# Kernel optimization log

Hardware: AMD Instinct MI355X
Metric: run time of the kernel (lower is better)

The kernel has to match this reference:

```python
import jax, jax.numpy as jnp
import numpy as np
import math

B, S, D, H, F = 4, 1024, 1024, 16, 4096
DH = D // H
NEG = -1000000.0  # matches masked_fill value in MaskedSoftmax
EPS = 1e-5        # torch LayerNorm default


def layer_norm(x, g, b):
    m = jnp.mean(x, axis=-1, keepdims=True)
    v = jnp.mean((x - m) ** 2, axis=-1, keepdims=True)
    return (x - m) * jax.lax.rsqrt(v + EPS) * g + b


def mha(q_in, k_in, v_in, Wq, bq, Wk, bk, Wv, bv, Wo, bo, mask):
    # mask: broadcastable to [B, H, Sq, Sk]; True = keep
    Bq, Sq, _ = q_in.shape
    Sk = k_in.shape[1]
    Q = (q_in @ Wq + bq).reshape(Bq, Sq, H, DH).transpose(0, 2, 1, 3)
    K = (k_in @ Wk + bk).reshape(Bq, Sk, H, DH).transpose(0, 2, 1, 3)
    V = (v_in @ Wv + bv).reshape(Bq, Sk, H, DH).transpose(0, 2, 1, 3)
    scores = jnp.einsum('bhqd,bhkd->bhqk', Q, K) / math.sqrt(DH)
    scores = jnp.where(mask, scores, NEG)
    A = jax.nn.softmax(scores, axis=-1)
    out = jnp.einsum('bhqk,bhkd->bhqd', A, V)
    out = out.transpose(0, 2, 1, 3).reshape(Bq, Sq, D)
    return out @ Wo + bo


def setup_inputs() -> dict:
    key = jax.random.key(0)
    ks = jax.random.split(key, 16)
    w = lambda k, shp: (jax.random.normal(k, shp, dtype=jnp.float32) * 0.02)
    inp = {
        'X': jax.random.normal(ks[0], (B, S, D), dtype=jnp.float32),
        'enc_outputs': jax.random.normal(ks[1], (B, S, D), dtype=jnp.float32),
        'enc_valid_lens': jax.random.randint(ks[2], (B,), 1, S + 1),
        # self-attention
        'Wq1': w(ks[3], (D, D)), 'bq1': jnp.zeros((D,), jnp.float32),
        'Wk1': w(ks[4], (D, D)), 'bk1': jnp.zeros((D,), jnp.float32),
        'Wv1': w(ks[5], (D, D)), 'bv1': jnp.zeros((D,), jnp.float32),
        'Wo1': w(ks[6], (D, D)), 'bo1': jnp.zeros((D,), jnp.float32),
        'g1': jnp.ones((D,), jnp.float32), 'be1': jnp.zeros((D,), jnp.float32),
        # cross-attention
        'Wq2': w(ks[7], (D, D)), 'bq2': jnp.zeros((D,), jnp.float32),
        'Wk2': w(ks[8], (D, D)), 'bk2': jnp.zeros((D,), jnp.float32),
        'Wv2': w(ks[9], (D, D)), 'bv2': jnp.zeros((D,), jnp.float32),
        'Wo2': w(ks[10], (D, D)), 'bo2': jnp.zeros((D,), jnp.float32),
        'g2': jnp.ones((D,), jnp.float32), 'be2': jnp.zeros((D,), jnp.float32),
        # FFN
        'Wf1': w(ks[11], (D, F)), 'bf1': jnp.zeros((F,), jnp.float32),
        'Wf2': w(ks[12], (F, D)), 'bf2': jnp.zeros((D,), jnp.float32),
        'g3': jnp.ones((D,), jnp.float32), 'be3': jnp.zeros((D,), jnp.float32),
    }
    return inp


def reference(X, enc_outputs, enc_valid_lens,
              Wq1, bq1, Wk1, bk1, Wv1, bv1, Wo1, bo1, g1, be1,
              Wq2, bq2, Wk2, bk2, Wv2, bv2, Wo2, bo2, g2, be2,
              Wf1, bf1, Wf2, bf2, g3, be3):
    # training mode, first decode step: key_values = X, causal dec mask
    idx = jnp.arange(S)
    causal = (idx[None, :] <= idx[:, None])[None, None]          # [1,1,S,S]
    cross = (idx[None, :] < enc_valid_lens[:, None])[:, None, None, :]  # [B,1,1,S]

    X2 = mha(X, X, X, Wq1, bq1, Wk1, bk1, Wv1, bv1, Wo1, bo1, causal)
    Y = layer_norm(X2 + X, g1, be1)
    Y2 = mha(Y, enc_outputs, enc_outputs, Wq2, bq2, Wk2, bk2, Wv2, bv2, Wo2, bo2, cross)
    Z = layer_norm(Y2 + Y, g2, be2)
    ffn = jax.nn.relu(Z @ Wf1 + bf1) @ Wf2 + bf2
    return layer_norm(ffn + Z, g3, be3)
```

## Files before the change

kernel.cpp:

```cpp
#include <hip/hip_runtime.h>
#include <stdint.h>

typedef unsigned short u16;
typedef __bf16 bf16x8 __attribute__((ext_vector_type(8)));
typedef float f32x4 __attribute__((ext_vector_type(4)));

#define BB 4
#define SS 1024
#define DD 1024
#define HH 16
#define DHH 64
#define FF 4096
#define NEGV -1000000.0f
#define LOG2E 1.4426950408889634f

__device__ __forceinline__ u16 f2b(float f) {
    uint32_t u = __float_as_uint(f);
    u += 0x7fff + ((u >> 16) & 1);
    return (u16)(u >> 16);
}
__device__ __forceinline__ float b2f(u16 u) {
    return __uint_as_float(((uint32_t)u) << 16);
}
__device__ __forceinline__ float exp2_raw(float x) {
    float r;
    asm volatile("v_exp_f32 %0, %1" : "=v"(r) : "v"(x));
    return r;
}
__device__ __forceinline__ void async16(const void* gp, void* lp) {
    auto g = reinterpret_cast<const __attribute__((address_space(1))) uint32_t*>(
        reinterpret_cast<uintptr_t>(gp));
    auto l = reinterpret_cast<__attribute__((address_space(3))) uint32_t*>(
        reinterpret_cast<uintptr_t>(lp));
    __builtin_amdgcn_global_load_lds(g, l, 16, 0, 0);
}

__global__ void cvt_bf16_kernel(const float* __restrict__ in, u16* __restrict__ out, int n4) {
    int i = blockIdx.x * blockDim.x + threadIdx.x;
    if (i >= n4) return;
    float4 v = reinterpret_cast<const float4*>(in)[i];
    ushort4 o;
    o.x = f2b(v.x); o.y = f2b(v.y); o.z = f2b(v.z); o.w = f2b(v.w);
    reinterpret_cast<ushort4*>(out)[i] = o;
}

__global__ void concat_bias_kernel(const float* __restrict__ a, const float* __restrict__ b,
                                   const float* __restrict__ c, float* __restrict__ out) {
    int i = blockIdx.x * 256 + threadIdx.x;
    float v;
    if (i < 1024) v = a[i];
    else if (i < 2048) v = b[i - 1024];
    else v = c[i - 2048];
    out[i] = v;
}

struct W8 { const float* p[8]; };
__global__ void wtrans8_kernel(W8 wp, u16* __restrict__ dst) {
    __shared__ u16 t[64][68];
    const float* W = wp.p[blockIdx.z];
    u16* Wt = dst + (size_t)blockIdx.z * 1024 * 1024;
    int n0 = blockIdx.x * 64, k0 = blockIdx.y * 64;
    int tx = threadIdx.x & 15, ty = threadIdx.x >> 4;
#pragma unroll
    for (int rr = 0; rr < 4; ++rr) {
        int r = ty + rr * 16;
        float4 v = *reinterpret_cast<const float4*>(&W[(size_t)(k0 + r) * 1024 + n0 + tx * 4]);
        ushort4 o;
        o.x = f2b(v.x); o.y = f2b(v.y); o.z = f2b(v.z); o.w = f2b(v.w);
        *reinterpret_cast<ushort4*>(&t[r][tx * 4]) = o;
    }
    __syncthreads();
#pragma unroll
    for (int rr = 0; rr < 4; ++rr) {
        int n = ty + rr * 16;
        ushort4 o;
        o.x = t[tx * 4 + 0][n];
        o.y = t[tx * 4 + 1][n];
        o.z = t[tx * 4 + 2][n];
        o.w = t[tx * 4 + 3][n];
        *reinterpret_cast<ushort4*>(&Wt[(size_t)(n0 + n) * 1024 + k0 + tx * 4]) = o;
    }
}

__global__ void wtrans_kernel(const float* __restrict__ W, u16* __restrict__ Wt, int K, int N) {
    __shared__ u16 t[64][68];
    int n0 = blockIdx.x * 64, k0 = blockIdx.y * 64;
    int tx = threadIdx.x & 15, ty = threadIdx.x >> 4;
#pragma unroll
    for (int rr = 0; rr < 4; ++rr) {
        int r = ty + rr * 16;
        float4 v = *reinterpret_cast<const float4*>(&W[(size_t)(k0 + r) * N + n0 + tx * 4]);
        ushort4 o;
        o.x = f2b(v.x); o.y = f2b(v.y); o.z = f2b(v.z); o.w = f2b(v.w);
        *reinterpret_cast<ushort4*>(&t[r][tx * 4]) = o;
    }
    __syncthreads();
#pragma unroll
    for (int rr = 0; rr < 4; ++rr) {
        int n = ty + rr * 16;
        ushort4 o;
        o.x = t[tx * 4 + 0][n];
        o.y = t[tx * 4 + 1][n];
        o.z = t[tx * 4 + 2][n];
        o.w = t[tx * 4 + 3][n];
        *reinterpret_cast<ushort4*>(&Wt[(size_t)(n0 + n) * K + k0 + tx * 4]) = o;
    }
}

__global__ void vtrans_kernel(const u16* __restrict__ V, int ldv, u16* __restrict__ VT) {
    __shared__ u16 t[32][33];
    int bh = blockIdx.z;
    int b = bh >> 4, h = bh & 15;
    int s0 = blockIdx.x * 32, d0 = blockIdx.y * 32;
    int tx = threadIdx.x, ty = threadIdx.y;
#pragma unroll
    for (int r = 0; r < 32; r += 8)
        t[ty + r][tx] = V[(size_t)(b * SS + s0 + ty + r) * ldv + h * DHH + d0 + tx];
    __syncthreads();
#pragma unroll
    for (int r = 0; r < 32; r += 8)
        VT[(size_t)(bh * DHH + d0 + ty + r) * SS + s0 + tx] = t[tx][ty + r];
}

template<int BM, bool OUT_BF16, bool RELU, int KSPLIT = 1>
__global__ __launch_bounds__(256, 3) void gemm_bt_kernel(
    const u16* __restrict__ A, const u16* __restrict__ Bt,
    const float* __restrict__ bias, void* __restrict__ Cv,
    int M, int N, int K, int qcols, float qscale)
{
    constexpr int MR = BM / 32;
    __shared__ __attribute__((aligned(16))) u16 As[BM][64];
    __shared__ __attribute__((aligned(16))) u16 Bs[128][64];
    const int tid = threadIdx.x;
    const int lane = tid & 63, wid = tid >> 6;
    const int wr = wid >> 1, wc = wid & 1;
    const int m0 = blockIdx.x * BM, n0 = blockIdx.y * 128;
    const int kz = (KSPLIT > 1) ? blockIdx.z : 0;
    const int Kc = K / KSPLIT;
    const int k0 = kz * Kc;
    const int arow = lane & 15;
    const int kseg = (lane >> 4) * 8;
    const int srow = lane >> 3;
    const int scol = ((lane & 7) ^ srow) * 8;
    const int rswz = (arow & 7) << 3;
    const f32x4 z4 = {0.f, 0.f, 0.f, 0.f};

    f32x4 acc[MR][4];
#pragma unroll
    for (int i = 0; i < MR; ++i)
#pragma unroll
        for (int j = 0; j < 4; ++j) acc[i][j] = z4;

    for (int kt = k0; kt < k0 + Kc; kt += 64) {
        __syncthreads();
#pragma unroll
        for (int i = 0; i < MR; ++i) {
            int ch = wid + i * 4;
            async16(&A[(size_t)(m0 + ch * 8 + srow) * K + kt + scol], &As[ch * 8][0]);
        }
#pragma unroll
        for (int i = 0; i < 4; ++i) {
            int ch = wid + i * 4;
            async16(&Bt[(size_t)(n0 + ch * 8 + srow) * K + kt + scol], &Bs[ch * 8][0]);
        }
        __syncthreads();
#pragma unroll
        for (int ks = 0; ks < 2; ++ks) {
            const int cswz = (ks * 32 + kseg) ^ rswz;
            bf16x8 af[MR], bfr[4];
#pragma unroll
            for (int mi = 0; mi < MR; ++mi)
                af[mi] = *reinterpret_cast<const bf16x8*>(&As[wr * (BM / 2) + mi * 16 + arow][cswz]);
#pragma unroll
            for (int ni = 0; ni < 4; ++ni)
                bfr[ni] = *reinterpret_cast<const bf16x8*>(&Bs[wc * 64 + ni * 16 + arow][cswz]);
#pragma unroll
            for (int mi = 0; mi < MR; ++mi)
#pragma unroll
                for (int ni = 0; ni < 4; ++ni)
                    acc[mi][ni] = __builtin_amdgcn_mfma_f32_16x16x32_bf16(af[mi], bfr[ni], acc[mi][ni], 0, 0, 0);
        }
    }
    const int rrow = (lane >> 4) * 4;
#pragma unroll
    for (int mi = 0; mi < MR; ++mi)
#pragma unroll
        for (int ni = 0; ni < 4; ++ni) {
            int col = n0 + wc * 64 + ni * 16 + arow;
            float bv = (kz == 0) ? bias[col] : 0.f;
            float sc = (col < qcols) ? qscale : 1.f;
#pragma unroll
            for (int r = 0; r < 4; ++r) {
                int row = m0 + wr * (BM / 2) + mi * 16 + rrow + r;
                float v = (acc[mi][ni][r] + bv) * sc;
                if (RELU) v = fmaxf(v, 0.f);
                size_t idx = (size_t)kz * M * N + (size_t)row * N + col;
                if (OUT_BF16) ((u16*)Cv)[idx] = f2b(v);
                else          ((float*)Cv)[idx] = v;
            }
        }
}

template<bool OUT_BF16, bool RELU, int KSPLIT = 1>
__global__ __launch_bounds__(512, 2) void gemm256_kernel(
    const u16* __restrict__ A, const u16* __restrict__ Bt,
    const float* __restrict__ bias, void* __restrict__ Cv,
    int M, int N, int K, int qcols, float qscale)
{
    __shared__ __attribute__((aligned(16))) u16 As[2][256][64];
    __shared__ __attribute__((aligned(16))) u16 Bs[2][256][64];
    const int tid = threadIdx.x, lane = tid & 63, wid = tid >> 6;
    const int wr = wid >> 2, wc = wid & 3;
    const int gx = gridDim.x, nwg = gridDim.x * gridDim.y;
    int bid = blockIdx.y * gx + blockIdx.x;
    int swz = (bid & 7) * (nwg >> 3) + (bid >> 3);
    const int m0 = (swz % gx) * 256, n0 = (swz / gx) * 256;
    const int kz = (KSPLIT > 1) ? blockIdx.z : 0;
    const int Kc = K / KSPLIT, k0 = kz * Kc, NT = Kc >> 6;
    const int a = lane & 15, g = lane >> 4;
    const int srow = lane >> 3;
    const int scol = ((lane & 7) ^ srow) * 8;
    const int rswz = (a & 7) << 3;
    const f32x4 z4 = {0.f, 0.f, 0.f, 0.f};

    f32x4 acc[8][4];
#pragma unroll
    for (int i = 0; i < 8; ++i)
#pragma unroll
        for (int j = 0; j < 4; ++j) acc[i][j] = z4;

    auto stageA = [&](int t, int h) {
        int kt = k0 + t * 64;
#pragma unroll
        for (int i = 0; i < 2; ++i) {
            int row = h * 128 + (wid * 2 + i) * 8;
            async16(&A[(size_t)(m0 + row + srow) * K + kt + scol], &As[t & 1][row][0]);
        }
    };
    auto stageB = [&](int t, int h) {
        int kt = k0 + t * 64;
#pragma unroll
        for (int i = 0; i < 2; ++i) {
            int row = h * 128 + (wid * 2 + i) * 8;
            async16(&Bt[(size_t)(n0 + row + srow) * K + kt + scol], &Bs[t & 1][row][0]);
        }
    };

    stageA(0, 0); stageA(0, 1); stageB(0, 0); stageB(0, 1);
    stageA(1, 0); stageA(1, 1); stageB(1, 0); stageB(1, 1);
    asm volatile("s_waitcnt vmcnt(8)" ::: "memory");
    __builtin_amdgcn_s_barrier();
    asm volatile("" ::: "memory");

    for (int t = 0; t < NT; ++t) {
        const int b = t & 1;
        bf16x8 bf[4][2];
#pragma unroll
        for (int p = 0; p < 4; ++p) {
            bf16x8 af[2][2];
#pragma unroll
            for (int m2 = 0; m2 < 2; ++m2)
#pragma unroll
                for (int ks = 0; ks < 2; ++ks)
                    af[m2][ks] = *reinterpret_cast<const bf16x8*>(
                        &As[b][wr * 128 + (p * 2 + m2) * 16 + a][(ks * 32 + g * 8) ^ rswz]);
            if (p == 0) {
#pragma unroll
                for (int ni = 0; ni < 4; ++ni)
#pragma unroll
                    for (int ks = 0; ks < 2; ++ks)
                        bf[ni][ks] = *reinterpret_cast<const bf16x8*>(
                            &Bs[b][wc * 64 + ni * 16 + a][(ks * 32 + g * 8) ^ rswz]);
            }
            if (p == 0 && t >= 1 && t + 1 < NT) stageA(t + 1, 0);
            if (p == 1 && t >= 1 && t + 1 < NT) stageA(t + 1, 1);
            if (p == 2 && t + 2 < NT) stageB(t + 2, 0);
            if (p == 3 && t + 2 < NT) stageB(t + 2, 1);
            asm volatile("" ::: "memory");
            __builtin_amdgcn_s_barrier();
            asm volatile("" ::: "memory");
            __builtin_amdgcn_s_setprio(1);
#pragma unroll
            for (int ks = 0; ks < 2; ++ks)
#pragma unroll
                for (int m2 = 0; m2 < 2; ++m2)
#pragma unroll
                    for (int ni = 0; ni < 4; ++ni)
                        acc[p * 2 + m2][ni] = __builtin_amdgcn_mfma_f32_16x16x32_bf16(
                            af[m2][ks], bf[ni][ks], acc[p * 2 + m2][ni], 0, 0, 0);
            __builtin_amdgcn_s_setprio(0);
        }
        if (t < NT - 1) {
            if (t < NT - 2) asm volatile("s_waitcnt vmcnt(4)" ::: "memory");
            else            asm volatile("s_waitcnt vmcnt(0)" ::: "memory");
            __builtin_amdgcn_s_barrier();
            asm volatile("" ::: "memory");
        }
    }

    const int rrow = g * 4;
#pragma unroll
    for (int mi = 0; mi < 8; ++mi)
#pragma unroll
        for (int ni = 0; ni < 4; ++ni) {
            int col = n0 + wc * 64 + ni * 16 + a;
            float bv = (kz == 0) ? bias[col] : 0.f;
            float sc = (col < qcols) ? qscale : 1.f;
#pragma unroll
            for (int r = 0; r < 4; ++r) {
                int row = m0 + wr * 128 + mi * 16 + rrow + r;
                float v = (acc[mi][ni][r] + bv) * sc;
                if (RELU) v = fmaxf(v, 0.f);
                size_t idx = (size_t)kz * M * N + (size_t)row * N + col;
                if (OUT_BF16) ((u16*)Cv)[idx] = f2b(v);
                else          ((float*)Cv)[idx] = v;
            }
        }
}

__global__ __launch_bounds__(512, 4) void flash_attn_kernel(
    const u16* __restrict__ Q, int ldq, const u16* __restrict__ Kp, int ldk,
    const u16* __restrict__ VT, u16* __restrict__ O,
    const int* __restrict__ vlens, int causal)
{
    __shared__ __attribute__((aligned(16))) u16 Ks[128][64];
    __shared__ __attribute__((aligned(16))) u16 Vs[64][128];
    __shared__ __attribute__((aligned(16))) u16 Ps[128][64];
    const int tid = threadIdx.x, lane = tid & 63, wid = tid >> 6;
    const int bh = blockIdx.x;
    int qb = blockIdx.y;
    if (causal) qb = (bh & 1) ? (7 - qb) : qb;
    const int b = bh >> 4, h = bh & 15;
    const int q0 = qb * 128;
    const int a = lane & 15;
    const int g = lane >> 4;
    const int kseg = g * 8;
    const int srow = lane >> 3;
    const int scol = ((lane & 7) ^ srow) * 8;
    const int vrow = lane >> 4;
    const int rswz = (a & 7) << 3;
    const int vswz = a << 3;
    const f32x4 z4 = {0.f, 0.f, 0.f, 0.f};

    bf16x8 qf[2];
#pragma unroll
    for (int ks = 0; ks < 2; ++ks)
        qf[ks] = *reinterpret_cast<const bf16x8*>(
            &Q[(size_t)(b * SS + q0 + wid * 16 + a) * ldq + h * DHH + ks * 32 + kseg]);

    float m_run = -3e38f, l_run = 0.f;
    f32x4 o[4];
#pragma unroll
    for (int nd = 0; nd < 4; ++nd) o[nd] = z4;

    int vl = causal ? SS : vlens[b];
    int ntiles = causal ? (qb + 1) : ((vl + 127) >> 7);

    for (int kt = 0; kt < ntiles; ++kt) {
        const int kv0 = kt * 128;
        __syncthreads();
#pragma unroll
        for (int i = 0; i < 2; ++i) {
            int ch = wid + i * 8;
            async16(&Kp[(size_t)(b * SS + kv0 + ch * 8 + srow) * ldk + h * DHH + scol], &Ks[ch * 8][0]);
            int cv = wid + i * 8;
            int vs = (cv * 4 + vrow) & 15;
            async16(&VT[(size_t)(bh * DHH + cv * 4 + vrow) * SS + kv0 + ((lane & 15) ^ vs) * 8], &Vs[cv * 4][0]);
        }
        __syncthreads();

        f32x4 st[8];
#pragma unroll
        for (int ni = 0; ni < 8; ++ni) st[ni] = z4;
        __builtin_amdgcn_s_setprio(1);
#pragma unroll
        for (int ks = 0; ks < 2; ++ks) {
            const int cswz = (ks * 32 + kseg) ^ rswz;
            bf16x8 kf[8];
#pragma unroll
            for (int ni = 0; ni < 8; ++ni)
                kf[ni] = *reinterpret_cast<const bf16x8*>(&Ks[ni * 16 + a][cswz]);
#pragma unroll
            for (int ni = 0; ni < 8; ++ni)
                st[ni] = __builtin_amdgcn_mfma_f32_16x16x32_bf16(kf[ni], qf[ks], st[ni], 0, 0, 0);
        }
        __builtin_amdgcn_s_setprio(0);

        bool domask = causal ? (kt == qb) : (kv0 + 128 > vl);
        if (domask) {
            const int qg = q0 + wid * 16 + a;
#pragma unroll
            for (int ni = 0; ni < 8; ++ni)
#pragma unroll
                for (int r = 0; r < 4; ++r) {
                    int cg = kv0 + ni * 16 + 4 * g + r;
                    bool keep = causal ? (cg <= qg) : (cg < vl);
                    if (!keep) st[ni][r] = NEGV;
                }
        }

        float tm = -3e38f;
#pragma unroll
        for (int ni = 0; ni < 8; ++ni)
#pragma unroll
            for (int r = 0; r < 4; ++r) tm = fmaxf(tm, st[ni][r]);
        tm = fmaxf(tm, __shfl_xor(tm, 16));
        tm = fmaxf(tm, __shfl_xor(tm, 32));
        bool need = __any(tm > m_run + 11.0f);
        float corr = 1.f;
        if (need) {
            float nm = fmaxf(m_run, tm);
            corr = exp2_raw(m_run - nm);
            m_run = nm;
        }
        float rs = 0.f;
#pragma unroll
        for (int ni = 0; ni < 8; ++ni)
#pragma unroll
            for (int r = 0; r < 4; ++r) {
                float p = exp2_raw(st[ni][r] - m_run);
                st[ni][r] = p;
                rs += p;
            }
        rs += __shfl_xor(rs, 16);
        rs += __shfl_xor(rs, 32);
        l_run = l_run * corr + rs;

        if (need) {
#pragma unroll
            for (int r = 0; r < 4; ++r) {
                float cr = __shfl(corr, (lane & 48) + 4 * g + r);
#pragma unroll
                for (int nd = 0; nd < 4; ++nd) o[nd][r] *= cr;
            }
        }

#pragma unroll
        for (int hh = 0; hh < 2; ++hh) {
#pragma unroll
            for (int ni4 = 0; ni4 < 4; ++ni4) {
                int ni = hh * 4 + ni4;
                uint2 pw;
                pw.x = (uint32_t)f2b(st[ni][0]) | ((uint32_t)f2b(st[ni][1]) << 16);
                pw.y = (uint32_t)f2b(st[ni][2]) | ((uint32_t)f2b(st[ni][3]) << 16);
                int prow = wid * 16 + a;
                int pcol = (ni4 * 16 + 4 * g) ^ rswz;
                *reinterpret_cast<uint2*>(&Ps[prow][pcol]) = pw;
            }
            __builtin_amdgcn_s_setprio(1);
#pragma unroll
            for (int kk = 0; kk < 2; ++kk) {
                const int kf_ = hh * 2 + kk;
                const int pswz = (kk * 32 + kseg) ^ rswz;
                const int cvswz = (kf_ * 32 + kseg) ^ vswz;
                bf16x8 pa, vb[4];
                pa = *reinterpret_cast<const bf16x8*>(&Ps[wid * 16 + a][pswz]);
#pragma unroll
                for (int nd = 0; nd < 4; ++nd)
                    vb[nd] = *reinterpret_cast<const bf16x8*>(&Vs[nd * 16 + a][cvswz]);
#pragma unroll
                for (int nd = 0; nd < 4; ++nd)
                    o[nd] = __builtin_amdgcn_mfma_f32_16x16x32_bf16(pa, vb[nd], o[nd], 0, 0, 0);
            }
            __builtin_amdgcn_s_setprio(0);
        }
    }

    float il = 1.f / l_run;
#pragma unroll
    for (int r = 0; r < 4; ++r) {
        float ilr = __shfl(il, (lane & 48) + 4 * g + r);
        int row = q0 + wid * 16 + 4 * g + r;
#pragma unroll
        for (int nd = 0; nd < 4; ++nd)
            O[(size_t)(b * SS + row) * DD + h * DHH + nd * 16 + a] = f2b(o[nd][r] * ilr);
    }
}

template<int NP>
__global__ void add_ln_kernel(const u16* __restrict__ P, size_t pstride,
                              const float* __restrict__ R,
                              const float* __restrict__ g, const float* __restrict__ be,
                              float* __restrict__ out32, u16* __restrict__ out16)
{
    __shared__ float red[4][2];
    const int row = blockIdx.x, tid = threadIdx.x;
    const size_t base = (size_t)row * DD;
    float4 vr = *reinterpret_cast<const float4*>(R + base + tid * 4);
    float x0 = vr.x, x1 = vr.y, x2 = vr.z, x3 = vr.w;
#pragma unroll
    for (int p = 0; p < NP; ++p) {
        ushort4 u = *reinterpret_cast<const ushort4*>(P + p * pstride + base + tid * 4);
        x0 += b2f(u.x); x1 += b2f(u.y); x2 += b2f(u.z); x3 += b2f(u.w);
    }
    float s = x0 + x1 + x2 + x3;
    float q = x0 * x0 + x1 * x1 + x2 * x2 + x3 * x3;
#pragma unroll
    for (int off = 32; off; off >>= 1) {
        s += __shfl_xor(s, off);
        q += __shfl_xor(q, off);
    }
    if ((tid & 63) == 0) { red[tid >> 6][0] = s; red[tid >> 6][1] = q; }
    __syncthreads();
    s = red[0][0] + red[1][0] + red[2][0] + red[3][0];
    q = red[0][1] + red[1][1] + red[2][1] + red[3][1];
    float mean = s * (1.f / 1024.f);
    float var = q * (1.f / 1024.f) - mean * mean;
    float rstd = rsqrtf(var + 1e-5f);
    int c = tid * 4;
    float o0 = (x0 - mean) * rstd * g[c + 0] + be[c + 0];
    float o1 = (x1 - mean) * rstd * g[c + 1] + be[c + 1];
    float o2 = (x2 - mean) * rstd * g[c + 2] + be[c + 2];
    float o3 = (x3 - mean) * rstd * g[c + 3] + be[c + 3];
    float4 ov = {o0, o1, o2, o3};
    *reinterpret_cast<float4*>(out32 + base + c) = ov;
    if (out16) {
        ushort4 hv;
        hv.x = f2b(o0); hv.y = f2b(o1); hv.z = f2b(o2); hv.w = f2b(o3);
        *reinterpret_cast<ushort4*>(out16 + base + c) = hv;
    }
}

extern "C" void kernel_launch(void* const* d_in, const int* in_sizes, int n_in,
                              void* d_out, int out_size, void* d_ws, size_t ws_size,
                              hipStream_t stream)
{
    const float* X   = (const float*)d_in[0];
    const float* ENC = (const float*)d_in[1];
    const int*   VL  = (const int*)d_in[2];
    const float* Wq1 = (const float*)d_in[3];  const float* bq1 = (const float*)d_in[4];
    const float* Wk1 = (const float*)d_in[5];  const float* bk1 = (const float*)d_in[6];
    const float* Wv1 = (const float*)d_in[7];  const float* bv1 = (const float*)d_in[8];
    const float* Wo1 = (const float*)d_in[9];  const float* bo1 = (const float*)d_in[10];
    const float* g1  = (const float*)d_in[11]; const float* be1 = (const float*)d_in[12];
    const float* Wq2 = (const float*)d_in[13]; const float* bq2 = (const float*)d_in[14];
    const float* Wk2 = (const float*)d_in[15]; const float* bk2 = (const float*)d_in[16];
    const float* Wv2 = (const float*)d_in[17]; const float* bv2 = (const float*)d_in[18];
    const float* Wo2 = (const float*)d_in[19]; const float* bo2 = (const float*)d_in[20];
    const float* g2  = (const float*)d_in[21]; const float* be2 = (const float*)d_in[22];
    const float* Wf1 = (const float*)d_in[23]; const float* bf1 = (const float*)d_in[24];
    const float* Wf2 = (const float*)d_in[25]; const float* bf2 = (const float*)d_in[26];
    const float* g3  = (const float*)d_in[27]; const float* be3 = (const float*)d_in[28];

    char* ws = (char*)d_ws;
    const size_t MB = 1024 * 1024;
    u16*   XBF  = (u16*)(ws + 0 * MB);
    u16*   ENCB = (u16*)(ws + 8 * MB);
    u16*   WTsq = (u16*)(ws + 16 * MB);
    u16*   WTf1 = (u16*)(ws + 32 * MB);
    u16*   WTf2 = (u16*)(ws + 40 * MB);
    u16*   QKV  = (u16*)(ws + 48 * MB);
    u16*   HF   = (u16*)(ws + 48 * MB);
    u16*   VTb  = (u16*)(ws + 80 * MB);
    u16*   AO   = (u16*)(ws + 88 * MB);
    u16*   P4   = (u16*)(ws + 80 * MB);
    u16*   P16  = (u16*)(ws + 96 * MB);
    float* Y32  = (float*)(ws + 112 * MB);
    u16*   YBF  = (u16*)(ws + 128 * MB);
    float* Z32  = (float*)(ws + 136 * MB);
    u16*   ZBF  = (u16*)(ws + 152 * MB);
    float* B1 = (float*)d_out;
    float* B2 = (float*)d_out + 4096;
    (void)ws_size; (void)in_sizes; (void)n_in; (void)out_size;

    const int M = BB * SS;
    const size_t MN = (size_t)M * DD;
    const float QS = 0.125f * LOG2E;

    cvt_bf16_kernel<<<M * DD / 4 / 256, 256, 0, stream>>>(X, XBF, M * DD / 4);
    cvt_bf16_kernel<<<M * DD / 4 / 256, 256, 0, stream>>>(ENC, ENCB, M * DD / 4);
    concat_bias_kernel<<<12, 256, 0, stream>>>(bq1, bk1, bv1, B1);
    concat_bias_kernel<<<8, 256, 0, stream>>>(bk2, bv2, bv2, B2);
    W8 w8 = {{Wq1, Wk1, Wv1, Wo1, Wq2, Wk2, Wv2, Wo2}};
    wtrans8_kernel<<<dim3(16, 16, 8), 256, 0, stream>>>(w8, WTsq);
    wtrans_kernel<<<dim3(64, 16), 256, 0, stream>>>(Wf1, WTf1, DD, FF);
    wtrans_kernel<<<dim3(16, 64), 256, 0, stream>>>(Wf2, WTf2, FF, DD);

    gemm256_kernel<true, false><<<dim3(16, 12), 512, 0, stream>>>(XBF, WTsq, B1, QKV, M, 3072, DD, 1024, QS);
    vtrans_kernel<<<dim3(32, 2, 64), dim3(32, 8), 0, stream>>>(QKV + 2048, 3072, VTb);
    flash_attn_kernel<<<dim3(64, 8), 512, 0, stream>>>(QKV, 3072, QKV + 1024, 3072, VTb, AO, VL, 1);
    gemm_bt_kernel<128, true, false, 2><<<dim3(32, 8, 2), 256, 0, stream>>>(AO, WTsq + 3u * 1024 * 1024, bo1, P16, M, DD, DD, 0, 1.f);
    add_ln_kernel<2><<<M, 256, 0, stream>>>(P16, MN, X, g1, be1, Y32, YBF);

    gemm_bt_kernel<64, true, false><<<dim3(64, 8), 256, 0, stream>>>(YBF, WTsq + 4u * 1024 * 1024, bq2, XBF, M, DD, DD, 1024, QS);
    gemm_bt_kernel<128, true, false><<<dim3(32, 16), 256, 0, stream>>>(ENCB, WTsq + 5u * 1024 * 1024, B2, QKV, M, 2048, DD, 0, 1.f);
    vtrans_kernel<<<dim3(32, 2, 64), dim3(32, 8), 0, stream>>>(QKV + 1024, 2048, VTb);
    flash_attn_kernel<<<dim3(64, 8), 512, 0, stream>>>(XBF, 1024, QKV, 2048, VTb, AO, VL, 0);
    gemm_bt_kernel<128, true, false, 2><<<dim3(32, 8, 2), 256, 0, stream>>>(AO, WTsq + 7u * 1024 * 1024, bo2, P16, M, DD, DD, 0, 1.f);
    add_ln_kernel<2><<<M, 256, 0, stream>>>(P16, MN, Y32, g2, be2, Z32, ZBF);

    gemm256_kernel<true, true><<<dim3(16, 16), 512, 0, stream>>>(ZBF, WTf1, bf1, HF, M, FF, DD, 0, 1.f);
    gemm256_kernel<true, false, 4><<<dim3(16, 4, 4), 512, 0, stream>>>(HF, WTf2, bf2, P4, M, DD, FF, 0, 1.f);
    add_ln_kernel<4><<<M, 256, 0, stream>>>(P4, MN, Z32, g3, be3, (float*)d_out, nullptr);
}
```

Before: 316.7 us.

## Restructure GEMM main loop into two-tile unrolled pipeline with explicit waits

Rewrites the 256x256 GEMM k-loop to process two k-tiles per iteration with eight phases. The schedule of async global-to-LDS loads changes: A is now staged one tile ahead and B two tiles ahead. An explicit lgkmcnt wait and sched_barrier come before the MFMAs, and a barrier follows every phase. The goal is to overlap loads with MFMA work better and to stop the compiler from interleaving LDS reads and MFMAs. The cost is more barriers per tile. Reusing the A buffer one tile ahead may also race, and NT must be even.

```diff
diff --git a/kernel.cpp b/kernel.cpp
--- a/kernel.cpp
+++ b/kernel.cpp
@@ -216,7 +216,7 @@
     int swz = (bid & 7) * (nwg >> 3) + (bid >> 3);
     const int m0 = (swz % gx) * 256, n0 = (swz / gx) * 256;
     const int kz = (KSPLIT > 1) ? blockIdx.z : 0;
-    const int Kc = K / KSPLIT, k0 = kz * Kc, NT = Kc >> 6;
+    const int Kc = K / KSPLIT, k0 = kz * Kc, NT = Kc >> 6, NI = NT >> 1;
     const int a = lane & 15, g = lane >> 4;
     const int srow = lane >> 3;
     const int scol = ((lane & 7) ^ srow) * 8;
@@ -247,52 +247,62 @@
     };
 
     stageA(0, 0); stageA(0, 1); stageB(0, 0); stageB(0, 1);
-    stageA(1, 0); stageA(1, 1); stageB(1, 0); stageB(1, 1);
-    asm volatile("s_waitcnt vmcnt(8)" ::: "memory");
+    stageB(1, 0); stageB(1, 1);
+    asm volatile("s_waitcnt vmcnt(4)" ::: "memory");
     __builtin_amdgcn_s_barrier();
     asm volatile("" ::: "memory");
 
-    for (int t = 0; t < NT; ++t) {
-        const int b = t & 1;
+    for (int i = 0; i < NI; ++i) {
+        const int t0 = 2 * i, t1 = 2 * i + 1;
         bf16x8 bf[4][2];
 #pragma unroll
-        for (int p = 0; p < 4; ++p) {
+        for (int p = 1; p <= 8; ++p) {
+            const int buf = (p > 4) ? 1 : 0;
+            const int q = (p - 1) & 3;
             bf16x8 af[2][2];
 #pragma unroll
             for (int m2 = 0; m2 < 2; ++m2)
 #pragma unroll
                 for (int ks = 0; ks < 2; ++ks)
                     af[m2][ks] = *reinterpret_cast<const bf16x8*>(
-                        &As[b][wr * 128 + (p * 2 + m2) * 16 + a][(ks * 32 + g * 8) ^ rswz]);
-            if (p == 0) {
+                        &As[buf][wr * 128 + (q * 2 + m2) * 16 + a][(ks * 32 + g * 8) ^ rswz]);
+            if (q == 0) {
 #pragma unroll
                 for (int ni = 0; ni < 4; ++ni)
 #pragma unroll
                     for (int ks = 0; ks < 2; ++ks)
                         bf[ni][ks] = *reinterpret_cast<const bf16x8*>(
-                            &Bs[b][wc * 64 + ni * 16 + a][(ks * 32 + g * 8) ^ rswz]);
-            }
-            if (p == 0 && t >= 1 && t + 1 < NT) stageA(t + 1, 0);
-            if (p == 1 && t >= 1 && t + 1 < NT) stageA(t + 1, 1);
-            if (p == 2 && t + 2 < NT) stageB(t + 2, 0);
-            if (p == 3 && t + 2 < NT) stageB(t + 2, 1);
+                            &Bs[buf][wc * 64 + ni * 16 + a][(ks * 32 + g * 8) ^ rswz]);
+            }
+            if (p == 1)                { stageA(t1, 0); stageA(t1, 1); }
+            if (p == 2 && t0 + 2 < NT) stageB(t0 + 2, 0);
+            if (p == 3 && t0 + 2 < NT) stageB(t0 + 2, 1);
+            if (p == 5 && t0 + 2 < NT) { stageA(t0 + 2, 0); stageA(t0 + 2, 1); }
+            if (p == 6 && t1 + 2 < NT) stageB(t1 + 2, 0);
+            if (p == 7 && t1 + 2 < NT) stageB(t1 + 2, 1);
             asm volatile("" ::: "memory");
             __builtin_amdgcn_s_barrier();
+            asm volatile("s_waitcnt lgkmcnt(0)" ::: "memory");
+            __builtin_amdgcn_sched_barrier(0);
+            __builtin_amdgcn_s_setprio(1);
+#pragma unroll
+            for (int ks = 0; ks < 2; ++ks)
+#pragma unroll
+                for (int m2 = 0; m2 < 2; ++m2)
+#pragma unroll
+                    for (int ni = 0; ni < 4; ++ni)
+                        acc[q * 2 + m2][ni] = __builtin_amdgcn_mfma_f32_16x16x32_bf16(
+                            af[m2][ks], bf[ni][ks], acc[q * 2 + m2][ni], 0, 0, 0);
+            __builtin_amdgcn_s_setprio(0);
+            if (p == 4) {
+                if (t0 + 2 < NT) asm volatile("s_waitcnt vmcnt(4)" ::: "memory");
+                else             asm volatile("s_waitcnt vmcnt(0)" ::: "memory");
+            }
+            if (p == 8) {
+                if (t1 + 2 < NT) asm volatile("s_waitcnt vmcnt(4)" ::: "memory");
+                else             asm volatile("s_waitcnt vmcnt(0)" ::: "memory");
+            }
             asm volatile("" ::: "memory");
-            __builtin_amdgcn_s_setprio(1);
-#pragma unroll
-            for (int ks = 0; ks < 2; ++ks)
-#pragma unroll
-                for (int m2 = 0; m2 < 2; ++m2)
-#pragma unroll
-                    for (int ni = 0; ni < 4; ++ni)
-                        acc[p * 2 + m2][ni] = __builtin_amdgcn_mfma_f32_16x16x32_bf16(
-                            af[m2][ks], bf[ni][ks], acc[p * 2 + m2][ni], 0, 0, 0);
-            __builtin_amdgcn_s_setprio(0);
-        }
-        if (t < NT - 1) {
-            if (t < NT - 2) asm volatile("s_waitcnt vmcnt(4)" ::: "memory");
-            else            asm volatile("s_waitcnt vmcnt(0)" ::: "memory");
             __builtin_amdgcn_s_barrier();
             asm volatile("" ::: "memory");
         }
```

New measurement: 325.5 us. +2.8%, slower.
